# Optimization experiments

Hardware: AMD Instinct MI355X
Metric: run time of the kernel (lower is better)

## Reference

```python
import jax, jax.numpy as jnp
import numpy as np

N, IN_F, OUT_F, HEADS = 4096, 512, 128, 8
ALPHA = 0.2
MASK_VAL = -9e15


def setup_inputs() -> dict:
    key = jax.random.key(0)
    k1, k2, k3, k4 = jax.random.split(key, 4)
    node_features = jax.random.normal(k1, (N, IN_F), dtype=jnp.float32)
    adj_matrix = jax.random.randint(k2, (N, N), 0, 2).astype(jnp.int32)
    # xavier_uniform-style scales
    w_lim = 1.414 * np.sqrt(6.0 / (IN_F + HEADS * OUT_F))
    a_lim = 1.414 * np.sqrt(6.0 / (2 * OUT_F + HEADS))
    W = jax.random.uniform(k3, (IN_F, HEADS * OUT_F), jnp.float32, -w_lim, w_lim)
    a = jax.random.uniform(k4, (2 * OUT_F, HEADS), jnp.float32, -a_lim, a_lim)
    return {"node_features": node_features, "adj_matrix": adj_matrix, "W": W, "a": a}


def reference(node_features, adj_matrix, W, a):
    n = node_features.shape[0]
    # (N, H, F) per-head projected features
    h = (node_features @ W).reshape(n, HEADS, OUT_F)
    # decompose e[i,j,h] = a_l . h_i + a_r . h_j (exactly equals the cat/matmul form)
    a_l, a_r = a[:OUT_F], a[OUT_F:]                      # (F, H) each
    left = jnp.einsum('nhf,fh->nh', h, a_l)              # (N, H)
    right = jnp.einsum('nhf,fh->nh', h, a_r)             # (N, H)
    e = left[:, None, :] + right[None, :, :]             # (N, N, H)
    e = jnp.where(e > 0, e, ALPHA * e)                   # LeakyReLU(alpha)
    e = jnp.where(adj_matrix[:, :, None] > 0, e, MASK_VAL)
    attn = jax.nn.softmax(e, axis=1)                     # softmax over source nodes j
    # dropout skipped (eval mode / rate 0.0)
    out = jnp.einsum('ijh,jhf->ihf', attn, h).reshape(n, HEADS * OUT_F)
    return jax.nn.elu(out)
```

## Files before the change

kernel.cpp:

```cpp
#include <hip/hip_runtime.h>
#include <stdint.h>

#define NN 4096
#define KIN 512
#define NH 8
#define DF 128
#define HID 1024

typedef __attribute__((ext_vector_type(8))) short bf16x8;
typedef __attribute__((ext_vector_type(4))) float f32x4;
typedef __attribute__((ext_vector_type(8))) unsigned short u16x8;
typedef __attribute__((ext_vector_type(4))) unsigned int u32x4;
typedef unsigned short u16;
typedef unsigned long long u64;

__device__ __forceinline__ u16 f2bf(float x){
  unsigned int u = __float_as_uint(x);
  return (u16)((u + 0x7fffu + ((u >> 16) & 1u)) >> 16);
}

__device__ __forceinline__ float fexp2(float x){
#if __has_builtin(__builtin_amdgcn_exp2f)
  return __builtin_amdgcn_exp2f(x);
#else
  return exp2f(x);
#endif
}

__device__ __forceinline__ void gload16(const void* g, void* lds){
  __builtin_amdgcn_global_load_lds(
      (const __attribute__((address_space(1))) unsigned int*)g,
      (__attribute__((address_space(3))) unsigned int*)lds, 16, 0, 0);
}

__global__ __launch_bounds__(256) void k_pack(const int* __restrict__ adj,
                                              unsigned long long* __restrict__ bm){
  int idx = blockIdx.x * 256 + threadIdx.x;
  int v = adj[idx] != 0;
  unsigned long long m = __ballot(v);
  if ((threadIdx.x & 63) == 0) bm[idx >> 6] = m;
}

__global__ __launch_bounds__(256) void k_conv(const float* __restrict__ X,
                                              const float* __restrict__ W,
                                              u16* __restrict__ A2,
                                              u16* __restrict__ WT){
  int idx = blockIdx.x * 256 + threadIdx.x;
  if (idx < NN * KIN) A2[idx] = f2bf(X[idx]);
  if (idx < HID * KIN){
    int n = idx / KIN, k = idx % KIN;
    WT[idx] = f2bf(W[k * HID + n]);
  }
}

__global__ __launch_bounds__(256) void k_gemm(const u16* __restrict__ A2,
                                              const u16* __restrict__ BT,
                                              float* __restrict__ C){
  __shared__ u16 As[8192], Bs[8192];
  const int tid = threadIdx.x;
  const int l = tid & 63, w = tid >> 6;
  const int wr = w >> 1, wc = w & 1;
  const int ib = blockIdx.x >> 3, nb = blockIdx.x & 7;
  const int p = l >> 4;
  f32x4 acc[4][4] = {};
  for (int k0 = 0; k0 < KIN; k0 += 64){
    __syncthreads();
    #pragma unroll
    for (int q = 0; q < 4; q++){
      int beta = ((q << 8) + tid) << 4;
      int row = beta >> 7, inner = beta & 127;
      int gin = inner ^ ((row & 7) << 4);
      gload16(A2 + (size_t)(ib * 128 + row) * KIN + k0 + (gin >> 1), (char*)As + beta);
      gload16(BT + (size_t)(nb * 128 + row) * KIN + k0 + (gin >> 1), (char*)Bs + beta);
    }
    __syncthreads();
    #pragma unroll
    for (int kk = 0; kk < 2; kk++){
      bf16x8 af[4], bfv[4];
      const int kb = ((kk << 5) + (p << 3)) << 1;
      #pragma unroll
      for (int m = 0; m < 4; m++){
        int r = wr * 64 + m * 16 + (l & 15);
        af[m] = *(const bf16x8*)((const char*)As + r * 128 + (kb ^ ((r & 7) << 4)));
      }
      #pragma unroll
      for (int n = 0; n < 4; n++){
        int r = wc * 64 + n * 16 + (l & 15);
        bfv[n] = *(const bf16x8*)((const char*)Bs + r * 128 + (kb ^ ((r & 7) << 4)));
      }
      #pragma unroll
      for (int m = 0; m < 4; m++)
        #pragma unroll
        for (int n = 0; n < 4; n++)
          acc[m][n] = __builtin_amdgcn_mfma_f32_16x16x32_bf16(af[m], bfv[n], acc[m][n], 0, 0, 0);
    }
  }
  #pragma unroll
  for (int m = 0; m < 4; m++)
    #pragma unroll
    for (int n = 0; n < 4; n++)
      #pragma unroll
      for (int r4 = 0; r4 < 4; r4++){
        int row = ib * 128 + wr * 64 + m * 16 + p * 4 + r4;
        int col = nb * 128 + wc * 64 + n * 16 + (l & 15);
        C[(size_t)row * HID + col] = acc[m][n][r4];
      }
}

__global__ __launch_bounds__(256) void k_lr(const float* __restrict__ h,
                                            const float* __restrict__ a,
                                            float* __restrict__ Lg,
                                            float* __restrict__ Rg){
  const int i = blockIdx.x;
  const int t = threadIdx.x;
  const int hd = t >> 5, l32 = t & 31;
  const int f = l32 << 2;
  const float4 hv = *(const float4*)(h + (size_t)i * HID + hd * DF + f);
  float pl = hv.x * a[(f + 0) * NH + hd] + hv.y * a[(f + 1) * NH + hd]
           + hv.z * a[(f + 2) * NH + hd] + hv.w * a[(f + 3) * NH + hd];
  float pr = hv.x * a[(128 + f + 0) * NH + hd] + hv.y * a[(128 + f + 1) * NH + hd]
           + hv.z * a[(128 + f + 2) * NH + hd] + hv.w * a[(128 + f + 3) * NH + hd];
  #pragma unroll
  for (int s = 1; s < 32; s <<= 1){
    pl += __shfl_xor(pl, s);
    pr += __shfl_xor(pr, s);
  }
  if (l32 == 0){
    int idx = hd * NN + i;
    Lg[idx] = pl * 1.44269504089f;
    Rg[idx] = pr * 1.44269504089f;
  }
}

__global__ __launch_bounds__(256) void k_tr(const float* __restrict__ h,
                                            u16* __restrict__ HT){
  __shared__ u16 T[64][80];
  const int it = blockIdx.x & 63, ft = blockIdx.x >> 6;
  const int i0 = it * 64, f0 = ft * 64;
  const int t = threadIdx.x;
  const int r = t >> 4, c = (t & 15) << 2;
  #pragma unroll
  for (int q = 0; q < 4; q++){
    int row = r + q * 16;
    float4 v = *(const float4*)(h + (size_t)(i0 + row) * HID + f0 + c);
    T[c + 0][row] = f2bf(v.x);
    T[c + 1][row] = f2bf(v.y);
    T[c + 2][row] = f2bf(v.z);
    T[c + 3][row] = f2bf(v.w);
  }
  __syncthreads();
  const int fr = t >> 2, c0 = (t & 3) << 4;
  u16x8 v0 = *(const u16x8*)&T[fr][c0];
  u16x8 v1 = *(const u16x8*)&T[fr][c0 + 8];
  *(u16x8*)(HT + (size_t)(f0 + fr) * NN + i0 + c0)     = v0;
  *(u16x8*)(HT + (size_t)(f0 + fr) * NN + i0 + c0 + 8) = v1;
}

__global__ __launch_bounds__(256) void k_agg(const u16* __restrict__ HT,
                                             const unsigned char* __restrict__ bm,
                                             const float* __restrict__ Lg,
                                             const float* __restrict__ Rg,
                                             float* __restrict__ P0,
                                             float* __restrict__ P1,
                                             float* __restrict__ D0,
                                             float* __restrict__ D1){
  __shared__ u16 Hs[2 * 8192];
  const int b = blockIdx.x;
  const int hd = b & 7;
  const int ib = (b >> 3) & 63;
  const int jh = b >> 9;
  const int i0 = ib * 64;
  const int jbase = jh * 2048;
  const int tid = threadIdx.x;
  const int w = tid >> 6, l = tid & 63;
  const int p = l >> 4;
  const int row_l = (w << 4) + (l & 15);
  const int gi = i0 + row_l;
  const float lgv = Lg[hd * NN + gi];
  const float* Rr = Rg + hd * NN;
  const u64* bmrow = (const u64*)(bm + (size_t)gi * 512);
  const u16* src = HT + (size_t)hd * DF * NN;
  f32x4 acc[8] = {};
  f32x4 accd = {};
  const short one_bf = (short)0x3F80;
  const bf16x8 ones = {one_bf, one_bf, one_bf, one_bf, one_bf, one_bf, one_bf, one_bf};

  auto stage = [&](int d, int j0s){
    #pragma unroll
    for (int q = 0; q < 4; q++){
      int beta = ((q << 8) + tid) << 4;
      int fr = beta >> 7, inner = beta & 127;
      int gin = inner ^ ((fr & 7) << 4);
      gload16(src + (size_t)fr * NN + j0s + (gin >> 1), (char*)Hs + d * 16384 + beta);
    }
  };

  stage(0, jbase);
  __syncthreads();

  for (int jt = 0; jt < 32; ++jt){
    const int j0 = jbase + (jt << 6);
    const int cur = jt & 1;
    if (jt < 31) stage(cur ^ 1, j0 + 64);

    const u64 bmv = bmrow[j0 >> 6];

    bf16x8 af[2];
    #pragma unroll
    for (int kk = 0; kk < 2; kk++){
      const int jb = j0 + (kk << 5) + (p << 3);
      const float4 rv0 = *(const float4*)(Rr + jb);
      const float4 rv1 = *(const float4*)(Rr + jb + 4);
      const unsigned int bbits = (unsigned int)(bmv >> (((kk << 2) + p) << 3)) & 0xffu;
      const float r8[8] = {rv0.x, rv0.y, rv0.z, rv0.w, rv1.x, rv1.y, rv1.z, rv1.w};
      float w8[8];
      #pragma unroll
      for (int e = 0; e < 8; e++){
        float s = lgv + r8[e];
        float t = fmaxf(s, 0.2f * s);
        t = ((bbits >> e) & 1u) ? t : -131072.f;
        w8[e] = fexp2(t);
      }
      unsigned int q0, q1, q2, q3;
      asm volatile("v_cvt_pk_bf16_f32 %0, %1, %2" : "=v"(q0) : "v"(w8[0]), "v"(w8[1]));
      asm volatile("v_cvt_pk_bf16_f32 %0, %1, %2" : "=v"(q1) : "v"(w8[2]), "v"(w8[3]));
      asm volatile("v_cvt_pk_bf16_f32 %0, %1, %2" : "=v"(q2) : "v"(w8[4]), "v"(w8[5]));
      asm volatile("v_cvt_pk_bf16_f32 %0, %1, %2" : "=v"(q3) : "v"(w8[6]), "v"(w8[7]));
      u32x4 uu = {q0, q1, q2, q3};
      af[kk] = __builtin_bit_cast(bf16x8, uu);
      accd = __builtin_amdgcn_mfma_f32_16x16x32_bf16(af[kk], ones, accd, 0, 0, 0);
    }

    const char* hb = (const char*)Hs + cur * 16384;
    #pragma unroll
    for (int kk = 0; kk < 2; kk++){
      const int kb = ((kk << 5) + (p << 3)) << 1;
      #pragma unroll
      for (int n = 0; n < 8; n++){
        const int fr = (n << 4) + (l & 15);
        bf16x8 bfr = *(const bf16x8*)(hb + fr * 128 + (kb ^ ((fr & 7) << 4)));
        acc[n] = __builtin_amdgcn_mfma_f32_16x16x32_bf16(af[kk], bfr, acc[n], 0, 0, 0);
      }
    }
    __syncthreads();
  }

  float* P = jh ? P1 : P0;
  float* D = jh ? D1 : D0;
  if ((l & 15) == 0){
    #pragma unroll
    for (int r4 = 0; r4 < 4; r4++)
      D[hd * NN + i0 + (w << 4) + (p << 2) + r4] = accd[r4];
  }

  const int rowbase = i0 + (w << 4) + (p << 2);
  #pragma unroll
  for (int r4 = 0; r4 < 4; r4++){
    const int grow = rowbase + r4;
    float* orow = P + (size_t)grow * HID + hd * DF;
    #pragma unroll
    for (int n = 0; n < 8; n++)
      orow[(n << 4) + (l & 15)] = acc[n][r4];
  }
}

__global__ __launch_bounds__(256) void k_comb(const float* __restrict__ P1,
                                              const float* __restrict__ D0,
                                              const float* __restrict__ D1,
                                              float* __restrict__ out){
  const int idx = blockIdx.x * 256 + threadIdx.x;
  const int i  = idx >> 8;
  const int c4 = idx & 255;
  const int hd = c4 >> 5;
  const float d = D0[hd * NN + i] + D1[hd * NN + i];
  const float rinv = 1.0f / d;
  float4 a0 = ((const float4*)out)[idx];
  float4 a1 = ((const float4*)P1)[idx];
  float4 v;
  v.x = (a0.x + a1.x) * rinv;
  v.y = (a0.y + a1.y) * rinv;
  v.z = (a0.z + a1.z) * rinv;
  v.w = (a0.w + a1.w) * rinv;
  v.x = v.x > 0.f ? v.x : (expf(v.x) - 1.0f);
  v.y = v.y > 0.f ? v.y : (expf(v.y) - 1.0f);
  v.z = v.z > 0.f ? v.z : (expf(v.z) - 1.0f);
  v.w = v.w > 0.f ? v.w : (expf(v.w) - 1.0f);
  ((float4*)out)[idx] = v;
}

extern "C" void kernel_launch(void* const* d_in, const int* in_sizes, int n_in,
                              void* d_out, int out_size, void* d_ws, size_t ws_size,
                              hipStream_t stream) {
  const float* X   = (const float*)d_in[0];
  const int*   adj = (const int*)d_in[1];
  const float* W   = (const float*)d_in[2];
  const float* a   = (const float*)d_in[3];
  float* out = (float*)d_out;

  char* ws = (char*)d_ws;
  size_t off = 0;
  float* h  = (float*)(ws + off);        off += (size_t)NN * HID * 4;
  u16*   A2 = (u16*)(ws + off);          off += (size_t)NN * KIN * 2;
  u16*   WT = (u16*)(ws + off);          off += (size_t)HID * KIN * 2;
  u16*   HT = (u16*)(ws + off);          off += (size_t)HID * NN * 2;
  unsigned char* bmp = (unsigned char*)(ws + off); off += (size_t)NN * 512;
  float* Lg = (float*)(ws + off);        off += (size_t)NH * NN * 4;
  float* Rg = (float*)(ws + off);        off += (size_t)NH * NN * 4;

  float* P0 = out;
  float* P1 = h;
  float* D0 = (float*)A2;
  float* D1 = D0 + NH * NN;

  k_pack<<<dim3(NN * NN / 256), dim3(256), 0, stream>>>(adj, (unsigned long long*)bmp);
  k_conv<<<dim3(NN * KIN / 256), dim3(256), 0, stream>>>(X, W, A2, WT);
  k_gemm<<<dim3(256), dim3(256), 0, stream>>>(A2, WT, h);
  k_lr  <<<dim3(NN), dim3(256), 0, stream>>>(h, a, Lg, Rg);
  k_tr  <<<dim3(1024), dim3(256), 0, stream>>>(h, HT);
  k_agg <<<dim3(1024), dim3(256), 0, stream>>>(HT, bmp, Lg, Rg, P0, P1, D0, D1);
  k_comb<<<dim3(NN * HID / 1024), dim3(256), 0, stream>>>(P1, D0, D1, out);
}
```

Baseline: 155.1 us.

## Split aggregation over four source-node quarters and vectorize adjacency bit packing

Result: faster. 146.0 us (-5.9%).

```diff
diff --git a/kernel.cpp b/kernel.cpp
--- a/kernel.cpp
+++ b/kernel.cpp
@@ -33,12 +33,15 @@
       (__attribute__((address_space(3))) unsigned int*)lds, 16, 0, 0);
 }
 
-__global__ __launch_bounds__(256) void k_pack(const int* __restrict__ adj,
-                                              unsigned long long* __restrict__ bm){
+__global__ __launch_bounds__(256) void k_pack(const int4* __restrict__ adj,
+                                              unsigned char* __restrict__ bm){
   int idx = blockIdx.x * 256 + threadIdx.x;
-  int v = adj[idx] != 0;
-  unsigned long long m = __ballot(v);
-  if ((threadIdx.x & 63) == 0) bm[idx >> 6] = m;
+  int4 a = adj[idx * 2];
+  int4 b = adj[idx * 2 + 1];
+  unsigned int m = (a.x != 0)        | ((a.y != 0) << 1) | ((a.z != 0) << 2) |
+                   ((a.w != 0) << 3) | ((b.x != 0) << 4) | ((b.y != 0) << 5) |
+                   ((b.z != 0) << 6) | ((b.w != 0) << 7);
+  bm[idx] = (unsigned char)m;
 }
 
 __global__ __launch_bounds__(256) void k_conv(const float* __restrict__ X,
@@ -156,21 +159,24 @@
   *(u16x8*)(HT + (size_t)(f0 + fr) * NN + i0 + c0 + 8) = v1;
 }
 
+template<int JSPLIT>
 __global__ __launch_bounds__(256) void k_agg(const u16* __restrict__ HT,
                                              const unsigned char* __restrict__ bm,
                                              const float* __restrict__ Lg,
                                              const float* __restrict__ Rg,
                                              float* __restrict__ P0,
                                              float* __restrict__ P1,
-                                             float* __restrict__ D0,
-                                             float* __restrict__ D1){
+                                             float* __restrict__ P2,
+                                             float* __restrict__ P3,
+                                             float* __restrict__ Dbase){
   __shared__ u16 Hs[2 * 8192];
   const int b = blockIdx.x;
   const int hd = b & 7;
   const int ib = (b >> 3) & 63;
-  const int jh = b >> 9;
+  const int jq = b >> 9;
   const int i0 = ib * 64;
-  const int jbase = jh * 2048;
+  const int jbase = jq * (NN / JSPLIT);
+  const int NT = (NN / JSPLIT) >> 6;
   const int tid = threadIdx.x;
   const int w = tid >> 6, l = tid & 63;
   const int p = l >> 4;
@@ -198,10 +204,10 @@
   stage(0, jbase);
   __syncthreads();
 
-  for (int jt = 0; jt < 32; ++jt){
+  for (int jt = 0; jt < NT; ++jt){
     const int j0 = jbase + (jt << 6);
     const int cur = jt & 1;
-    if (jt < 31) stage(cur ^ 1, j0 + 64);
+    if (jt < NT - 1) stage(cur ^ 1, j0 + 64);
 
     const u64 bmv = bmrow[j0 >> 6];
 
@@ -245,8 +251,8 @@
     __syncthreads();
   }
 
-  float* P = jh ? P1 : P0;
-  float* D = jh ? D1 : D0;
+  float* P = (jq == 0) ? P0 : (jq == 1) ? P1 : (jq == 2) ? P2 : P3;
+  float* D = Dbase + jq * NH * NN;
   if ((l & 15) == 0){
     #pragma unroll
     for (int r4 = 0; r4 < 4; r4++)
@@ -264,23 +270,29 @@
   }
 }
 
+template<int JS>
 __global__ __launch_bounds__(256) void k_comb(const float* __restrict__ P1,
-                                              const float* __restrict__ D0,
-                                              const float* __restrict__ D1,
+                                              const float* __restrict__ P2,
+                                              const float* __restrict__ P3,
+                                              const float* __restrict__ Db,
                                               float* __restrict__ out){
   const int idx = blockIdx.x * 256 + threadIdx.x;
   const int i  = idx >> 8;
   const int c4 = idx & 255;
   const int hd = c4 >> 5;
-  const float d = D0[hd * NN + i] + D1[hd * NN + i];
+  float d = Db[hd * NN + i] + Db[NH * NN + hd * NN + i];
+  if (JS == 4) d += Db[2 * NH * NN + hd * NN + i] + Db[3 * NH * NN + hd * NN + i];
   const float rinv = 1.0f / d;
   float4 a0 = ((const float4*)out)[idx];
   float4 a1 = ((const float4*)P1)[idx];
   float4 v;
-  v.x = (a0.x + a1.x) * rinv;
-  v.y = (a0.y + a1.y) * rinv;
-  v.z = (a0.z + a1.z) * rinv;
-  v.w = (a0.w + a1.w) * rinv;
+  v.x = a0.x + a1.x; v.y = a0.y + a1.y; v.z = a0.z + a1.z; v.w = a0.w + a1.w;
+  if (JS == 4){
+    float4 a2 = ((const float4*)P2)[idx];
+    float4 a3 = ((const float4*)P3)[idx];
+    v.x += a2.x + a3.x; v.y += a2.y + a3.y; v.z += a2.z + a3.z; v.w += a2.w + a3.w;
+  }
+  v.x *= rinv; v.y *= rinv; v.z *= rinv; v.w *= rinv;
   v.x = v.x > 0.f ? v.x : (expf(v.x) - 1.0f);
   v.y = v.y > 0.f ? v.y : (expf(v.y) - 1.0f);
   v.z = v.z > 0.f ? v.z : (expf(v.z) - 1.0f);
@@ -306,17 +318,26 @@
   unsigned char* bmp = (unsigned char*)(ws + off); off += (size_t)NN * 512;
   float* Lg = (float*)(ws + off);        off += (size_t)NH * NN * 4;
   float* Rg = (float*)(ws + off);        off += (size_t)NH * NN * 4;
+  float* P2 = (float*)(ws + off);
+  float* P3 = P2 + (size_t)NN * HID;
+  const size_t need4 = off + 2 * (size_t)NN * HID * 4;
 
   float* P0 = out;
   float* P1 = h;
-  float* D0 = (float*)A2;
-  float* D1 = D0 + NH * NN;
-
-  k_pack<<<dim3(NN * NN / 256), dim3(256), 0, stream>>>(adj, (unsigned long long*)bmp);
+  float* Db = (float*)A2;
+
+  const bool quarters = ws_size >= need4;
+
+  k_pack<<<dim3(NN * NN / 8 / 256), dim3(256), 0, stream>>>((const int4*)adj, bmp);
   k_conv<<<dim3(NN * KIN / 256), dim3(256), 0, stream>>>(X, W, A2, WT);
   k_gemm<<<dim3(256), dim3(256), 0, stream>>>(A2, WT, h);
   k_lr  <<<dim3(NN), dim3(256), 0, stream>>>(h, a, Lg, Rg);
   k_tr  <<<dim3(1024), dim3(256), 0, stream>>>(h, HT);
-  k_agg <<<dim3(1024), dim3(256), 0, stream>>>(HT, bmp, Lg, Rg, P0, P1, D0, D1);
-  k_comb<<<dim3(NN * HID / 1024), dim3(256), 0, stream>>>(P1, D0, D1, out);
-}
+  if (quarters){
+    k_agg<4><<<dim3(2048), dim3(256), 0, stream>>>(HT, bmp, Lg, Rg, P0, P1, P2, P3, Db);
+    k_comb<4><<<dim3(NN * HID / 1024), dim3(256), 0, stream>>>(P1, P2, P3, Db, out);
+  } else {
+    k_agg<2><<<dim3(1024), dim3(256), 0, stream>>>(HT, bmp, Lg, Rg, P0, P1, P2, P3, Db);
+    k_comb<2><<<dim3(NN * HID / 1024), dim3(256), 0, stream>>>(P1, P2, P3, Db, out);
+  }
+}
```
